# Kernel tuning notes

Hardware: AMD Instinct MI355X
Metric: run time of the kernel (lower is better)

The kernel has to match this reference:

```python
import jax, jax.numpy as jnp
import numpy as np


def setup_inputs() -> dict:
    key = jax.random.key(0)
    k1, k2 = jax.random.split(key)
    N, M, D = 8192, 8192, 64
    X1 = jax.random.normal(k1, (N, D), dtype=jnp.float32)
    X2 = jax.random.normal(k2, (M, D), dtype=jnp.float32)
    l = jnp.float32(1.0)
    sigma_f = jnp.float32(1.0)
    return {"X1": X1, "X2": X2, "l": l, "sigma_f": sigma_f}


def reference(X1, X2, l, sigma_f):
    sq1 = jnp.sum(X1 * X1, axis=1)               # [N]
    sq2 = jnp.sum(X2 * X2, axis=1)               # [M]
    cross = jnp.einsum("nd,md->nm", X1, X2)      # [N,M] GEMM
    dist = sq1[:, None] + sq2[None, :] - 2.0 * cross
    dist = jnp.maximum(dist, 0.0)                # clamp numerical negatives
    return sigma_f ** 2 * jnp.exp(-0.5 * dist / l ** 2)
```

## Files before the change

kernel.cpp:

```cpp
#include <hip/hip_runtime.h>
#include <hip/hip_bf16.h>

#define DD 64
#define TN 128
#define TM 256

typedef short short8 __attribute__((ext_vector_type(8)));
typedef unsigned short us8 __attribute__((ext_vector_type(8)));
typedef float f32x4 __attribute__((ext_vector_type(4)));

__device__ __forceinline__ float bf2f(unsigned short h) {
    union { unsigned u; float f; } v; v.u = ((unsigned)h) << 16;
    return v.f;
}
__device__ __forceinline__ unsigned short f2bf(float x) {
    __hip_bfloat16 b = __float2bfloat16(x);
    unsigned short u;
    __builtin_memcpy(&u, &b, 2);
    return u;
}

__global__ __launch_bounds__(256, 2) void sqexp_kernel(
    const float* __restrict__ X1, const float* __restrict__ X2,
    const float* __restrict__ lp, const float* __restrict__ sfp,
    float* __restrict__ out, int N, int M)
{
    __shared__ __align__(16) unsigned char ldsbuf[TM * DD * 2 * 2];
    __shared__ float sq1[TN];
    __shared__ float sq2[TM];

    unsigned short* Bh = (unsigned short*)ldsbuf;
    unsigned short* Bl = (unsigned short*)(ldsbuf + TM * DD * 2);

    const int t    = threadIdx.x;
    const int w    = t >> 6;
    const int lane = t & 63;
    const int n0   = blockIdx.y * TN;
    const int m0   = blockIdx.x * TM;

    const int wr = (w >> 1) * 64;
    const int wc = (w & 1) * 128;

    {
        const float4* Bp = (const float4*)(X2 + (size_t)(m0 + t) * DD);
        float4 bv[16];
        #pragma unroll
        for (int j = 0; j < 16; ++j) bv[j] = Bp[j];

        float s2 = 0.0f;
        #pragma unroll
        for (int c = 0; c < 8; ++c) {
            float4 f0 = bv[2 * c], f1 = bv[2 * c + 1];
            float xs[8] = { f0.x, f0.y, f0.z, f0.w, f1.x, f1.y, f1.z, f1.w };
            us8 hv, lv;
            #pragma unroll
            for (int e = 0; e < 8; ++e) {
                s2 = fmaf(xs[e], xs[e], s2);
                unsigned short h = f2bf(xs[e]);
                hv[e] = h;
                lv[e] = f2bf(xs[e] - bf2f(h));
            }
            int byte = t * 128 + ((c * 16) ^ ((t & 7) << 4));
            *(us8*)&Bh[byte >> 1] = hv;
            *(us8*)&Bl[byte >> 1] = lv;
        }
        sq2[t] = s2;
    }

    short8 ah[4][2], al[4][2];
    #pragma unroll
    for (int fm = 0; fm < 4; ++fm) {
        const int row = n0 + wr + fm * 16 + (lane & 15);
        const float4* Ap = (const float4*)(X1 + (size_t)row * DD) + (lane >> 4) * 2;
        float p = 0.0f;
        #pragma unroll
        for (int ks = 0; ks < 2; ++ks) {
            float4 f0 = Ap[ks * 8];
            float4 f1 = Ap[ks * 8 + 1];
            float xs[8] = { f0.x, f0.y, f0.z, f0.w, f1.x, f1.y, f1.z, f1.w };
            us8 hv, lv;
            #pragma unroll
            for (int e = 0; e < 8; ++e) {
                p = fmaf(xs[e], xs[e], p);
                unsigned short h = f2bf(xs[e]);
                hv[e] = h;
                lv[e] = f2bf(xs[e] - bf2f(h));
            }
            __builtin_memcpy(&ah[fm][ks], &hv, 16);
            __builtin_memcpy(&al[fm][ks], &lv, 16);
        }
        p += __shfl_xor(p, 16);
        p += __shfl_xor(p, 32);
        if ((w & 1) == 0 && (lane >> 4) == 0) sq1[wr + fm * 16 + lane] = p;
    }
    __syncthreads();

    f32x4 acc[4][8] = {};
    #pragma unroll
    for (int ks = 0; ks < 2; ++ks) {
        #pragma unroll
        for (int fn = 0; fn < 8; ++fn) {
            int brow = wc + fn * 16 + (lane & 15);
            int byte = brow * 128 + (((ks * 64) + (lane >> 4) * 16) ^ ((brow & 7) << 4));
            short8 bh = *(const short8*)&Bh[byte >> 1];
            short8 bl = *(const short8*)&Bl[byte >> 1];
            #pragma unroll
            for (int fm = 0; fm < 4; ++fm) {
                acc[fm][fn] = __builtin_amdgcn_mfma_f32_16x16x32_bf16(bh, ah[fm][ks], acc[fm][fn], 0, 0, 0);
                acc[fm][fn] = __builtin_amdgcn_mfma_f32_16x16x32_bf16(bl, ah[fm][ks], acc[fm][fn], 0, 0, 0);
                acc[fm][fn] = __builtin_amdgcn_mfma_f32_16x16x32_bf16(bh, al[fm][ks], acc[fm][fn], 0, 0, 0);
            }
        }
    }
    __syncthreads();

    const float lv_ = lp[0], sf = sfp[0];
    const float c1  = -0.5f / (lv_ * lv_);
    const float cm2 = -2.0f * c1;
    const float amp = sf * sf;

    float a1[4];
    #pragma unroll
    for (int fm = 0; fm < 4; ++fm) a1[fm] = c1 * sq1[wr + fm * 16 + (lane & 15)];

    #pragma unroll
    for (int p = 0; p < 2; ++p) {
        if ((w >> 1) == p) {
            #pragma unroll
            for (int fn = 0; fn < 8; ++fn) {
                f32x4 s  = *(const f32x4*)&sq2[wc + fn * 16 + (lane >> 4) * 4];
                f32x4 a2 = c1 * s;
                #pragma unroll
                for (int fm = 0; fm < 4; ++fm) {
                    f32x4 o;
                    #pragma unroll
                    for (int r = 0; r < 4; ++r) {
                        float arg = fminf(fmaf(cm2, acc[fm][fn][r], a1[fm] + a2[r]), 0.0f);
                        o[r] = amp * __expf(arg);
                    }
                    int R = fm * 16 + (lane & 15);
                    int C = wc + fn * 16 + (lane >> 4) * 4;
                    *(f32x4*)(ldsbuf + R * 1024 + ((C * 4) ^ ((R & 7) << 4))) = o;
                }
            }
        }
        __syncthreads();

        #pragma unroll
        for (int i = 0; i < 16; ++i) {
            int R = w * 16 + i;
            f32x4 v = *(const f32x4*)(ldsbuf + R * 1024 + ((lane ^ (R & 7)) * 16));
            size_t off = (size_t)(n0 + p * 64 + R) * M + m0 + 4 * lane;
            *(f32x4*)&out[off] = v;
        }
        __syncthreads();
    }
}

extern "C" void kernel_launch(void* const* d_in, const int* in_sizes, int n_in,
                              void* d_out, int out_size, void* d_ws, size_t ws_size,
                              hipStream_t stream) {
    const float* X1 = (const float*)d_in[0];
    const float* X2 = (const float*)d_in[1];
    const float* lp = (const float*)d_in[2];
    const float* sf = (const float*)d_in[3];
    float* out = (float*)d_out;
    const int N = in_sizes[0] / DD;
    const int M = in_sizes[1] / DD;
    dim3 grid(M / TM, N / TN);
    sqexp_kernel<<<grid, 256, 0, stream>>>(X1, X2, lp, sf, out, N, M);
}
```

Baseline: 78.12 us.

## Retile to 256x128 blocks with 512 threads, swizzled block order, nontemporal stores

Changes the block tile from 128x256 to 256x128, runs 8 waves per block with each wave owning a 64x64 sub-tile, and uses a 1D grid remapped into patches tuned for cache locality (chiplet-aware ordering). Row norms for X1 now stay in registers instead of shared memory. The output is staged through a separate LDS buffer and written with nontemporal stores. The block-index mapping hard-codes the grid shape and assumes 32x64 tiles (N=M=8192), so other sizes would map blocks incorrectly.

```diff
diff --git a/kernel.cpp b/kernel.cpp
--- a/kernel.cpp
+++ b/kernel.cpp
@@ -2,8 +2,8 @@
 #include <hip/hip_bf16.h>
 
 #define DD 64
-#define TN 128
-#define TM 256
+#define TN 256
+#define TM 128
 
 typedef short short8 __attribute__((ext_vector_type(8)));
 typedef unsigned short us8 __attribute__((ext_vector_type(8)));
@@ -20,37 +20,50 @@
     return u;
 }
 
-__global__ __launch_bounds__(256, 2) void sqexp_kernel(
+__global__ __launch_bounds__(512, 2) void sqexp_kernel(
     const float* __restrict__ X1, const float* __restrict__ X2,
     const float* __restrict__ lp, const float* __restrict__ sfp,
     float* __restrict__ out, int N, int M)
 {
-    __shared__ __align__(16) unsigned char ldsbuf[TM * DD * 2 * 2];
-    __shared__ float sq1[TN];
+    __shared__ __align__(16) unsigned char Bbuf[TM * DD * 2 * 2];
+    __shared__ __align__(16) unsigned char Obuf[64 * 512];
     __shared__ float sq2[TM];
 
-    unsigned short* Bh = (unsigned short*)ldsbuf;
-    unsigned short* Bl = (unsigned short*)(ldsbuf + TM * DD * 2);
+    unsigned short* Bh = (unsigned short*)Bbuf;
+    unsigned short* Bl = (unsigned short*)(Bbuf + TM * DD * 2);
 
     const int t    = threadIdx.x;
     const int w    = t >> 6;
     const int lane = t & 63;
-    const int n0   = blockIdx.y * TN;
-    const int m0   = blockIdx.x * TM;
+    const int wr   = (w >> 1) * 64;
+    const int wc   = (w & 1) * 64;
 
-    const int wr = (w >> 1) * 64;
-    const int wc = (w & 1) * 128;
+    const int F      = blockIdx.x;
+    const int k      = F & 7;
+    const int l      = F >> 3;
+    const int patch  = l >> 5;
+    const int within = l & 31;
+    const int bx     = k * 8 + (patch & 1) * 4 + (within & 3);
+    const int by     = (patch >> 1) * 8 + (within >> 2);
+    const int n0     = by * TN;
+    const int m0     = bx * TM;
+
+    const float lv_ = lp[0], sf = sfp[0];
+    const float c1  = -0.5f / (lv_ * lv_);
+    const float cm2 = -2.0f * c1;
+    const float amp = sf * sf;
 
     {
-        const float4* Bp = (const float4*)(X2 + (size_t)(m0 + t) * DD);
-        float4 bv[16];
+        const int row = t >> 2, q = t & 3;
+        const float4* Bp = (const float4*)(X2 + (size_t)(m0 + row) * DD) + q * 4;
+        float4 f[4];
         #pragma unroll
-        for (int j = 0; j < 16; ++j) bv[j] = Bp[j];
+        for (int j = 0; j < 4; ++j) f[j] = Bp[j];
 
         float s2 = 0.0f;
         #pragma unroll
-        for (int c = 0; c < 8; ++c) {
-            float4 f0 = bv[2 * c], f1 = bv[2 * c + 1];
+        for (int c = 0; c < 2; ++c) {
+            float4 f0 = f[2 * c], f1 = f[2 * c + 1];
             float xs[8] = { f0.x, f0.y, f0.z, f0.w, f1.x, f1.y, f1.z, f1.w };
             us8 hv, lv;
             #pragma unroll
@@ -60,14 +73,17 @@
                 hv[e] = h;
                 lv[e] = f2bf(xs[e] - bf2f(h));
             }
-            int byte = t * 128 + ((c * 16) ^ ((t & 7) << 4));
+            int byte = row * 128 + (((q * 2 + c) * 16) ^ ((row & 7) << 4));
             *(us8*)&Bh[byte >> 1] = hv;
             *(us8*)&Bl[byte >> 1] = lv;
         }
-        sq2[t] = s2;
+        s2 += __shfl_xor(s2, 1);
+        s2 += __shfl_xor(s2, 2);
+        if (q == 0) sq2[row] = s2;
     }
 
     short8 ah[4][2], al[4][2];
+    float a1[4];
     #pragma unroll
     for (int fm = 0; fm < 4; ++fm) {
         const int row = n0 + wr + fm * 16 + (lane & 15);
@@ -91,15 +107,15 @@
         }
         p += __shfl_xor(p, 16);
         p += __shfl_xor(p, 32);
-        if ((w & 1) == 0 && (lane >> 4) == 0) sq1[wr + fm * 16 + lane] = p;
+        a1[fm] = c1 * p;
     }
     __syncthreads();
 
-    f32x4 acc[4][8] = {};
+    f32x4 acc[4][4] = {};
     #pragma unroll
     for (int ks = 0; ks < 2; ++ks) {
         #pragma unroll
-        for (int fn = 0; fn < 8; ++fn) {
+        for (int fn = 0; fn < 4; ++fn) {
             int brow = wc + fn * 16 + (lane & 15);
             int byte = brow * 128 + (((ks * 64) + (lane >> 4) * 16) ^ ((brow & 7) << 4));
             short8 bh = *(const short8*)&Bh[byte >> 1];
@@ -112,22 +128,12 @@
             }
         }
     }
-    __syncthreads();
-
-    const float lv_ = lp[0], sf = sfp[0];
-    const float c1  = -0.5f / (lv_ * lv_);
-    const float cm2 = -2.0f * c1;
-    const float amp = sf * sf;
-
-    float a1[4];
-    #pragma unroll
-    for (int fm = 0; fm < 4; ++fm) a1[fm] = c1 * sq1[wr + fm * 16 + (lane & 15)];
 
     #pragma unroll
-    for (int p = 0; p < 2; ++p) {
+    for (int p = 0; p < 4; ++p) {
         if ((w >> 1) == p) {
             #pragma unroll
-            for (int fn = 0; fn < 8; ++fn) {
+            for (int fn = 0; fn < 4; ++fn) {
                 f32x4 s  = *(const f32x4*)&sq2[wc + fn * 16 + (lane >> 4) * 4];
                 f32x4 a2 = c1 * s;
                 #pragma unroll
@@ -140,18 +146,19 @@
                     }
                     int R = fm * 16 + (lane & 15);
                     int C = wc + fn * 16 + (lane >> 4) * 4;
-                    *(f32x4*)(ldsbuf + R * 1024 + ((C * 4) ^ ((R & 7) << 4))) = o;
+                    *(f32x4*)(Obuf + R * 512 + ((C * 4) ^ ((R & 7) << 4))) = o;
                 }
             }
         }
         __syncthreads();
 
         #pragma unroll
-        for (int i = 0; i < 16; ++i) {
-            int R = w * 16 + i;
-            f32x4 v = *(const f32x4*)(ldsbuf + R * 1024 + ((lane ^ (R & 7)) * 16));
-            size_t off = (size_t)(n0 + p * 64 + R) * M + m0 + 4 * lane;
-            *(f32x4*)&out[off] = v;
+        for (int i = 0; i < 4; ++i) {
+            int R = w * 8 + i * 2 + (lane >> 5);
+            int c = lane & 31;
+            f32x4 v = *(const f32x4*)(Obuf + R * 512 + ((c ^ (R & 7)) * 16));
+            size_t off = (size_t)(n0 + p * 64 + R) * M + m0 + 4 * c;
+            __builtin_nontemporal_store(v, (f32x4*)&out[off]);
         }
         __syncthreads();
     }
@@ -167,6 +174,6 @@
     float* out = (float*)d_out;
     const int N = in_sizes[0] / DD;
     const int M = in_sizes[1] / DD;
-    dim3 grid(M / TM, N / TN);
-    sqexp_kernel<<<grid, 256, 0, stream>>>(X1, X2, lp, sf, out, N, M);
+    const int nblk = (N / TN) * (M / TM);
+    sqexp_kernel<<<nblk, 512, 0, stream>>>(X1, X2, lp, sf, out, N, M);
 }
```

Measured after the change: 95.82 us. 22.7% more time.
